# Performance work log

Hardware: AMD Instinct MI355X
Metric: run time of the kernel (lower is better)

## Reference

```python
import jax, jax.numpy as jnp
import numpy as np

ALPHA, BETA, K_CONST, N = 0.0001, 0.75, 2.0, 5


def setup_inputs() -> dict:
    key = jax.random.key(0)
    x = jax.random.normal(key, (16, 256, 256, 96), dtype=jnp.float32)
    return {"x": x}


def reference(x):
    # Faithful to the keras LRNLayer: for each channel i the layer computes a
    # GLOBAL scalar sq_i = sum over (batch, H, W, channel-window) of x**2,
    # window = [max(0, int(i - n/2)), min(nc-1, i + int(n/2)) + 1).
    # With n=5, int(i - 2.5) truncates toward zero -> lo = max(0, i - 3);
    # hi = min(nc-1, i+2) + 1.  Then out[..., i] = x[..., i] / (k + alpha*sq_i)**beta.
    nc = x.shape[-1]
    # per-channel energy over batch/H/W -> [C]
    e = jnp.sum(x * x, axis=(0, 1, 2))
    # inclusive prefix sum with leading zero for O(1) window sums
    cs = jnp.concatenate([jnp.zeros((1,), dtype=e.dtype), jnp.cumsum(e)])  # [C+1]
    i = jnp.arange(nc)
    lo = jnp.maximum(0, i - 3)               # matches int() truncation for n=5
    hi = jnp.minimum(nc - 1, i + 2) + 1
    sq = cs[hi] - cs[lo]                     # [C] windowed sum of squares
    denom = (K_CONST + ALPHA * sq) ** BETA   # [C]
    return x / denom                         # broadcast over trailing channel dim
```

## Files before the change

kernel.cpp:

```cpp
#include <hip/hip_runtime.h>


typedef float f32x4 __attribute__((ext_vector_type(4)));

#define R_TOTAL (16 * 256 * 256)
#define C 96
#define C4 24
#define GRID 2048
#define BLK 384
#define NSLAB 32
#define HEAD_SLABS 18

__global__ void lrn_zero(float* __restrict__ e) {
    if (threadIdx.x < C) e[threadIdx.x] = 0.0f;
}

__global__ __launch_bounds__(BLK) void lrn_reduce(const f32x4* __restrict__ x4,
                                                  float* __restrict__ e) {
    __shared__ float se[C];
    const int tid = threadIdx.x;
    if (tid < C) se[tid] = 0.0f;
    __syncthreads();

    const int c4 = tid % C4;
    const int rowoff = tid / C4;
    float a0 = 0.f, a1 = 0.f, a2 = 0.f, a3 = 0.f;

    const int stride = GRID * 16;
    const int rbase = blockIdx.x * 16 + rowoff;

    for (int k = 0; k < HEAD_SLABS; ++k) {
        f32x4 v = x4[(k * stride + rbase) * C4 + c4];
        a0 += v.x * v.x; a1 += v.y * v.y; a2 += v.z * v.z; a3 += v.w * v.w;
    }
    for (int k = HEAD_SLABS; k < NSLAB; ++k) {
        f32x4 v = __builtin_nontemporal_load(&x4[(k * stride + rbase) * C4 + c4]);
        a0 += v.x * v.x; a1 += v.y * v.y; a2 += v.z * v.z; a3 += v.w * v.w;
    }

    const int c0 = c4 * 4;
    atomicAdd(&se[c0 + 0], a0);
    atomicAdd(&se[c0 + 1], a1);
    atomicAdd(&se[c0 + 2], a2);
    atomicAdd(&se[c0 + 3], a3);
    __syncthreads();
    if (tid < C) atomicAdd(&e[tid], se[tid]);
}

__global__ __launch_bounds__(BLK) void lrn_scale(const f32x4* __restrict__ x4,
                                                  f32x4* __restrict__ o4,
                                                  const float* __restrict__ e) {
    __shared__ float se[C];
    __shared__ float sinv[C];
    const int tid = threadIdx.x;
    if (tid < C) se[tid] = e[tid];
    __syncthreads();
    if (tid < C) {
        const int lo = (tid - 3 < 0) ? 0 : tid - 3;
        const int hi = (tid + 2 > C - 1) ? C - 1 : tid + 2;
        float s = 0.f;
        for (int j = lo; j <= hi; ++j) s += se[j];
        sinv[tid] = powf(2.0f + 1.0e-4f * s, -0.75f);
    }
    __syncthreads();

    const int c4 = tid % C4;
    const int rowoff = tid / C4;
    const int c0 = c4 * 4;
    const float s0 = sinv[c0 + 0];
    const float s1 = sinv[c0 + 1];
    const float s2 = sinv[c0 + 2];
    const float s3 = sinv[c0 + 3];

    const int stride = GRID * 16;
    const int rbase = blockIdx.x * 16 + rowoff;

    for (int k = 0; k < HEAD_SLABS; ++k) {
        const int idx = (k * stride + rbase) * C4 + c4;
        f32x4 v = x4[idx];
        v.x *= s0; v.y *= s1; v.z *= s2; v.w *= s3;
        __builtin_nontemporal_store(v, &o4[idx]);
    }
    for (int k = HEAD_SLABS; k < NSLAB; ++k) {
        const int idx = (k * stride + rbase) * C4 + c4;
        f32x4 v = __builtin_nontemporal_load(&x4[idx]);
        v.x *= s0; v.y *= s1; v.z *= s2; v.w *= s3;
        __builtin_nontemporal_store(v, &o4[idx]);
    }
}

extern "C" void kernel_launch(void* const* d_in, const int* in_sizes, int n_in,
                              void* d_out, int out_size, void* d_ws, size_t ws_size,
                              hipStream_t stream) {
    const f32x4* x4 = (const f32x4*)d_in[0];
    f32x4* o4 = (f32x4*)d_out;
    float* e = (float*)d_ws;

    lrn_zero<<<1, 128, 0, stream>>>(e);
    lrn_reduce<<<GRID, BLK, 0, stream>>>(x4, e);
    lrn_scale<<<GRID, BLK, 0, stream>>>(x4, o4, e);
}
```

Baseline: 213.9 us.

## Fuse reduce and scale into one cooperative kernel with register and cache reuse

Replaces the separate zero, reduce and scale launches with a single cooperative kernel that uses grid-wide syncs between phases. Each thread keeps its first 24 float4 loads in registers. The scale pass walks the later half of the data in reverse so that recently read lines may still be in L2 or the last-level cache, which is meant to cut the second full read of the 400MB input. The channel partial sums are spread over 8 global slots to reduce atomic contention. The cost is higher register pressure, lower occupancy because the grid is capped at 512 blocks, and two grid barriers. The old three-kernel path remains as a fallback if the cooperative launch fails.

```diff
diff --git a/kernel.cpp b/kernel.cpp
--- a/kernel.cpp
+++ b/kernel.cpp
@@ -1,18 +1,129 @@
 #include <hip/hip_runtime.h>
+#include <hip/hip_cooperative_groups.h>
+
+namespace cg = cooperative_groups;
 
 
 typedef float f32x4 __attribute__((ext_vector_type(4)));
 
-#define R_TOTAL (16 * 256 * 256)
 #define C 96
 #define C4 24
-#define GRID 2048
 #define BLK 384
+#define MAXGRID 512
+#define TOTAL_F4 25165824
+#define SW_R 24
+#define NPART 8
+
+__global__ __launch_bounds__(BLK, 3) void lrn_fused(const f32x4* __restrict__ x4,
+                                                    f32x4* __restrict__ o4,
+                                                    float* __restrict__ ep) {
+    const int tid = threadIdx.x;
+    const int nt = gridDim.x * BLK;
+    const int g = blockIdx.x * BLK + tid;
+    const int c0 = (g % C4) * 4;
+    const int nsweep = TOTAL_F4 / nt;
+    const int rem = TOTAL_F4 - nsweep * nt;
+    const int hstart = nsweep - nsweep / 2;
+    __shared__ float se[C];
+    __shared__ float sinv[C];
+    if (tid < C) se[tid] = 0.0f;
+    if (blockIdx.x < NPART && tid < C)
+        __hip_atomic_store(&ep[blockIdx.x * C + tid], 0.0f,
+                           __ATOMIC_RELAXED, __HIP_MEMORY_SCOPE_AGENT);
+
+    cg::this_grid().sync();
+
+    float a0 = 0.f, a1 = 0.f, a2 = 0.f, a3 = 0.f;
+    f32x4 r[SW_R];
+
+    #pragma unroll
+    for (int s = 0; s < SW_R; ++s) {
+        f32x4 v = __builtin_nontemporal_load(&x4[s * nt + g]);
+        r[s] = v;
+        a0 += v.x * v.x; a1 += v.y * v.y; a2 += v.z * v.z; a3 += v.w * v.w;
+    }
+    #pragma unroll 4
+    for (int s = SW_R; s < hstart; ++s) {
+        f32x4 v = __builtin_nontemporal_load(&x4[s * nt + g]);
+        a0 += v.x * v.x; a1 += v.y * v.y; a2 += v.z * v.z; a3 += v.w * v.w;
+    }
+    #pragma unroll 4
+    for (int s = hstart; s < nsweep; ++s) {
+        f32x4 v = x4[s * nt + g];
+        a0 += v.x * v.x; a1 += v.y * v.y; a2 += v.z * v.z; a3 += v.w * v.w;
+    }
+    if (g < rem) {
+        f32x4 v = x4[nsweep * nt + g];
+        a0 += v.x * v.x; a1 += v.y * v.y; a2 += v.z * v.z; a3 += v.w * v.w;
+    }
+
+    atomicAdd(&se[c0 + 0], a0);
+    atomicAdd(&se[c0 + 1], a1);
+    atomicAdd(&se[c0 + 2], a2);
+    atomicAdd(&se[c0 + 3], a3);
+    __syncthreads();
+    if (tid < C)
+        atomicAdd(&ep[(blockIdx.x & (NPART - 1)) * C + tid], se[tid]);
+    __threadfence();
+
+    cg::this_grid().sync();
+
+    if (tid < C) {
+        float t = 0.f;
+        #pragma unroll
+        for (int p = 0; p < NPART; ++p)
+            t += __hip_atomic_load(&ep[p * C + tid],
+                                   __ATOMIC_RELAXED, __HIP_MEMORY_SCOPE_AGENT);
+        se[tid] = t;
+    }
+    __syncthreads();
+    if (tid < C) {
+        const int lo = (tid - 3 < 0) ? 0 : tid - 3;
+        const int hi = (tid + 2 > C - 1) ? C - 1 : tid + 2;
+        float s = 0.f;
+        for (int j = lo; j <= hi; ++j) s += se[j];
+        sinv[tid] = powf(2.0f + 1.0e-4f * s, -0.75f);
+    }
+    __syncthreads();
+    const float s0 = sinv[c0 + 0];
+    const float s1 = sinv[c0 + 1];
+    const float s2 = sinv[c0 + 2];
+    const float s3 = sinv[c0 + 3];
+
+    #pragma unroll 4
+    for (int s = nsweep - 1; s >= hstart; --s) {
+        const int idx = s * nt + g;
+        f32x4 v = x4[idx];
+        v.x *= s0; v.y *= s1; v.z *= s2; v.w *= s3;
+        __builtin_nontemporal_store(v, &o4[idx]);
+    }
+    if (g < rem) {
+        const int idx = nsweep * nt + g;
+        f32x4 v = x4[idx];
+        v.x *= s0; v.y *= s1; v.z *= s2; v.w *= s3;
+        __builtin_nontemporal_store(v, &o4[idx]);
+    }
+    #pragma unroll
+    for (int s = 0; s < SW_R; ++s) {
+        f32x4 v = r[s];
+        v.x *= s0; v.y *= s1; v.z *= s2; v.w *= s3;
+        __builtin_nontemporal_store(v, &o4[s * nt + g]);
+    }
+    #pragma unroll 4
+    for (int s = SW_R; s < hstart; ++s) {
+        const int idx = s * nt + g;
+        f32x4 v = __builtin_nontemporal_load(&x4[idx]);
+        v.x *= s0; v.y *= s1; v.z *= s2; v.w *= s3;
+        __builtin_nontemporal_store(v, &o4[idx]);
+    }
+}
+
+#define FGRID 2048
 #define NSLAB 32
 #define HEAD_SLABS 18
 
 __global__ void lrn_zero(float* __restrict__ e) {
-    if (threadIdx.x < C) e[threadIdx.x] = 0.0f;
+    if (threadIdx.x < NPART * C) e[threadIdx.x] = 0.0f;
 }
 
 __global__ __launch_bounds__(BLK) void lrn_reduce(const f32x4* __restrict__ x4,
@@ -21,14 +132,11 @@
     const int tid = threadIdx.x;
     if (tid < C) se[tid] = 0.0f;
     __syncthreads();
-
     const int c4 = tid % C4;
     const int rowoff = tid / C4;
     float a0 = 0.f, a1 = 0.f, a2 = 0.f, a3 = 0.f;
-
-    const int stride = GRID * 16;
+    const int stride = FGRID * 16;
     const int rbase = blockIdx.x * 16 + rowoff;
-
     for (int k = 0; k < HEAD_SLABS; ++k) {
         f32x4 v = x4[(k * stride + rbase) * C4 + c4];
         a0 += v.x * v.x; a1 += v.y * v.y; a2 += v.z * v.z; a3 += v.w * v.w;
@@ -37,7 +145,6 @@
         f32x4 v = __builtin_nontemporal_load(&x4[(k * stride + rbase) * C4 + c4]);
         a0 += v.x * v.x; a1 += v.y * v.y; a2 += v.z * v.z; a3 += v.w * v.w;
     }
-
     const int c0 = c4 * 4;
     atomicAdd(&se[c0 + 0], a0);
     atomicAdd(&se[c0 + 1], a1);
@@ -63,18 +170,13 @@
         sinv[tid] = powf(2.0f + 1.0e-4f * s, -0.75f);
     }
     __syncthreads();
-
     const int c4 = tid % C4;
     const int rowoff = tid / C4;
     const int c0 = c4 * 4;
-    const float s0 = sinv[c0 + 0];
-    const float s1 = sinv[c0 + 1];
-    const float s2 = sinv[c0 + 2];
-    const float s3 = sinv[c0 + 3];
-
-    const int stride = GRID * 16;
+    const float s0 = sinv[c0 + 0], s1 = sinv[c0 + 1];
+    const float s2 = sinv[c0 + 2], s3 = sinv[c0 + 3];
+    const int stride = FGRID * 16;
     const int rbase = blockIdx.x * 16 + rowoff;
-
     for (int k = 0; k < HEAD_SLABS; ++k) {
         const int idx = (k * stride + rbase) * C4 + c4;
         f32x4 v = x4[idx];
@@ -94,9 +196,21 @@
                               hipStream_t stream) {
     const f32x4* x4 = (const f32x4*)d_in[0];
     f32x4* o4 = (f32x4*)d_out;
-    float* e = (float*)d_ws;
-
-    lrn_zero<<<1, 128, 0, stream>>>(e);
-    lrn_reduce<<<GRID, BLK, 0, stream>>>(x4, e);
-    lrn_scale<<<GRID, BLK, 0, stream>>>(x4, o4, e);
-}
+    float* ep = (float*)d_ws;
+
+    int maxB = 0;
+    hipError_t qe = hipOccupancyMaxActiveBlocksPerMultiprocessor(&maxB, lrn_fused, BLK, 0);
+    hipError_t le = hipErrorUnknown;
+    if (qe == hipSuccess && maxB >= 1) {
+        int grid = maxB * 256;
+        if (grid > MAXGRID) grid = MAXGRID;
+        void* args[] = {(void*)&x4, (void*)&o4, (void*)&ep};
+        le = hipLaunchCooperativeKernel((void*)lrn_fused, dim3(grid), dim3(BLK),
+                                        args, 0, stream);
+    }
+    if (le != hipSuccess) {
+        lrn_zero<<<1, NPART * C, 0, stream>>>(ep);
+        lrn_reduce<<<FGRID, BLK, 0, stream>>>(x4, ep);
+        lrn_scale<<<FGRID, BLK, 0, stream>>>(x4, o4, ep);
+    }
+}
```

Result: no change. 210.2 us (-1.7%).
